# Kernel tuning notes

Measured on AMD Instinct MI355X. Metric: run time of the kernel, lower is better.

## Reference

```python
import jax, jax.numpy as jnp
import numpy as np

KERNEL_NUM = 21
SIGMA = 0.1
EXACT_SIGMA = 0.001

def _kernel_params():
    mus, sigs = [], []
    for i in range(KERNEL_NUM):
        mu = 1.0 / (KERNEL_NUM - 1) + 2.0 * i / (KERNEL_NUM - 1) - 1.0
        s = SIGMA
        if mu > 1:
            mu = 1.0
            s = EXACT_SIGMA
        mus.append(mu)
        sigs.append(s)
    return np.array(mus, np.float32), np.array(sigs, np.float32)

MUS, SIGS = _kernel_params()

def _l2norm(x):
    # torch F.normalize(p=2, dim=-1): x / max(||x||, 1e-12)
    n = jnp.sqrt(jnp.sum(x * x, axis=-1, keepdims=True))
    return x / jnp.maximum(n, 1e-12)

def setup_inputs() -> dict:
    key = jax.random.key(0)
    ks = jax.random.split(key, 8)
    B, W, R, D, V = 512, 30, 512, 128, 100000
    H1, H2 = 128, 64
    return {
        "query": jax.random.randint(ks[0], (B, W), 0, V),
        "document": jax.random.randint(ks[1], (B, R), 0, V),
        "emb_table": jax.random.normal(ks[2], (V, D), jnp.float32) * 0.02,
        "w1": jax.random.normal(ks[3], (KERNEL_NUM, H1), jnp.float32) * 0.1,
        "b1": jnp.zeros((H1,), jnp.float32),
        "w2": jax.random.normal(ks[4], (H1, H2), jnp.float32) * 0.1,
        "b2": jnp.zeros((H2,), jnp.float32),
        "w3": jax.random.normal(ks[5], (H2, 1), jnp.float32) * 0.1,
        "b3": jnp.zeros((1,), jnp.float32),
    }

def reference(query, document, emb_table, w1, b1, w2, b2, w3, b3):
    q = _l2norm(emb_table[query])      # [B, W, D]
    d = _l2norm(emb_table[document])   # [B, R, D]
    # cosine matching matrix [B, W, R]
    M = jnp.einsum('bwd,brd->bwr', q, d)
    # 21 Gaussian soft-histogram bins: log1p(sum_{w,r} exp(-0.5*(M-mu)^2/sigma^2))
    KM = [
        jnp.log1p(
            jnp.sum(jnp.exp(-0.5 * (M - MUS[i]) ** 2 / (SIGS[i] ** 2)), axis=(-1, -2))
        )
        for i in range(KERNEL_NUM)
    ]
    k = jnp.stack(KM, axis=1)  # [B, K]
    h = jax.nn.relu(k @ w1 + b1)
    h = jax.nn.relu(h @ w2 + b2)
    return h @ w3 + b3  # [B, 1]
```

## Files before the change

kernel.cpp:

```cpp
#include <hip/hip_runtime.h>
#include <math.h>

#define B_   512
#define W_   30
#define R_   512
#define D_   128
#define NK_  21
#define SPLIT 4
#define QSTRIDE 132

typedef __attribute__((ext_vector_type(8))) short  bf16x8;
typedef __attribute__((ext_vector_type(4))) float  f32x4;
typedef __attribute__((ext_vector_type(2))) float  f32x2;

__device__ __forceinline__ unsigned short f2bf(float f) {
    union { float f; unsigned int u; } v; v.f = f;
    unsigned int u = v.u;
    return (unsigned short)((u + 0x7fffu + ((u >> 16) & 1u)) >> 16);
}

__device__ __forceinline__ float fast_exp2(float x) {
#if __has_builtin(__builtin_amdgcn_exp2f)
    return __builtin_amdgcn_exp2f(x);
#else
    float r; asm volatile("v_exp_f32 %0, %1" : "=v"(r) : "v"(x)); return r;
#endif
}

#define QROWS 32
#define QST   136

__global__ __launch_bounds__(512) void knrm_bins_kernel(
    const int* __restrict__ query, const int* __restrict__ doc,
    const float* __restrict__ emb,
    float* __restrict__ part)
{
    const int bid  = blockIdx.x;
    const int b    = ((bid >> 5) << 3) | (bid & 7);
    const int sp   = (bid >> 3) & 3;
    const int tid  = threadIdx.x;
    const int lane = tid & 63;
    const int wid  = tid >> 6;
    const int l15  = lane & 15;
    const int lhi  = lane >> 4;

    __shared__ unsigned short qlds[QROWS * QST];
    __shared__ float wred8[8][NK_][8];

    const int di = doc[b * R_ + sp * 128 + wid * 16 + l15];
    const float* drow = emb + (size_t)di * D_ + lhi * 8;
    float4 f[8];
    #pragma unroll
    for (int kk = 0; kk < 4; ++kk) {
        f[2 * kk]     = *(const float4*)(drow + kk * 32);
        f[2 * kk + 1] = *(const float4*)(drow + kk * 32 + 4);
    }

    {
        int w = tid >> 4, j = tid & 15;
        uint4 o4 = make_uint4(0, 0, 0, 0);
        if (w < W_) {
            int qi = query[b * W_ + w];
            const float* qrow = emb + (size_t)qi * D_ + j * 8;
            float4 qa = *(const float4*)(qrow);
            float4 qb = *(const float4*)(qrow + 4);
            float ss = qa.x*qa.x + qa.y*qa.y + qa.z*qa.z + qa.w*qa.w
                     + qb.x*qb.x + qb.y*qb.y + qb.z*qb.z + qb.w*qb.w;
            #pragma unroll
            for (int off = 8; off >= 1; off >>= 1) ss += __shfl_xor(ss, off, 16);
            float qinv = 1.0f / fmaxf(sqrtf(ss), 1e-12f);
            unsigned short o[8];
            o[0] = f2bf(qa.x*qinv); o[1] = f2bf(qa.y*qinv);
            o[2] = f2bf(qa.z*qinv); o[3] = f2bf(qa.w*qinv);
            o[4] = f2bf(qb.x*qinv); o[5] = f2bf(qb.y*qinv);
            o[6] = f2bf(qb.z*qinv); o[7] = f2bf(qb.w*qinv);
            o4 = *(const uint4*)o;
        }
        *(uint4*)(&qlds[(tid >> 4) * QST + (tid & 15) * 8]) = o4;
    }

    float nsq = 0.f;
    #pragma unroll
    for (int c = 0; c < 8; ++c)
        nsq = fmaf(f[c].x, f[c].x, fmaf(f[c].y, f[c].y,
              fmaf(f[c].z, f[c].z, fmaf(f[c].w, f[c].w, nsq))));
    nsq += __shfl_xor(nsq, 16, 64);
    nsq += __shfl_xor(nsq, 32, 64);
    const float dinv = 1.0f / fmaxf(sqrtf(nsq), 1e-12f);

    bf16x8 a[4];
    #pragma unroll
    for (int kk = 0; kk < 4; ++kk) {
        float4 u = f[2 * kk], v = f[2 * kk + 1];
        unsigned short o[8];
        o[0] = f2bf(u.x*dinv); o[1] = f2bf(u.y*dinv);
        o[2] = f2bf(u.z*dinv); o[3] = f2bf(u.w*dinv);
        o[4] = f2bf(v.x*dinv); o[5] = f2bf(v.y*dinv);
        o[6] = f2bf(v.z*dinv); o[7] = f2bf(v.w*dinv);
        a[kk] = *(const bf16x8*)o;
    }
    __syncthreads();

    bf16x8 bq[2][4];
    #pragma unroll
    for (int tc = 0; tc < 2; ++tc)
        #pragma unroll
        for (int kk = 0; kk < 4; ++kk)
            bq[tc][kk] = *(const bf16x8*)&qlds[(tc * 16 + l15) * QST + kk * 32 + lhi * 8];

    f32x4 acc0 = (f32x4)0.0f, acc1 = (f32x4)0.0f;
    #pragma unroll
    for (int kk = 0; kk < 4; ++kk) {
        acc0 = __builtin_amdgcn_mfma_f32_16x16x32_bf16(a[kk], bq[0][kk], acc0, 0, 0, 0);
        acc1 = __builtin_amdgcn_mfma_f32_16x16x32_bf16(a[kk], bq[1][kk], acc1, 0, 0, 0);
    }

    const float CW = -72.134752f;
    const float CE = -721347.52f;
    const float RC = 0.36787944f;

    f32x2 kacc2[NK_];
    #pragma unroll
    for (int i = 0; i < NK_; ++i) kacc2[i] = (f32x2)0.0f;

    #pragma unroll
    for (int p = 0; p < 4; ++p) {
        f32x2 mm;
        mm.x = acc0[p];
        mm.y = (l15 < 14) ? acc1[p] : 3.0f;
        f32x2 t0 = mm + 0.95f;

        #pragma unroll
        for (int g = 0; g < 3; ++g) {
            const int   gs = (g == 0) ? 0 : (g == 1) ? 7 : 14;
            const int   gl = (g == 2) ? 6 : 7;
            const float go = 0.1f * (float)gs;
            f32x2 tg = t0 - go;
            f32x2 e  = (CW * tg) * tg;
            f32x2 dl = 14.4269504f * tg - 0.72134752f;
            f32x2 R, r;
            R.x = fast_exp2(e.x);  R.y = fast_exp2(e.y);
            r.x = fast_exp2(dl.x); r.y = fast_exp2(dl.y);
            #pragma unroll
            for (int k = 0; k < 7; ++k) {
                if (k < gl) {
                    kacc2[gs + k] += R;
                    R *= r;
                    r *= RC;
                }
            }
        }

        f32x2 y = mm - 1.0f;
        f32x2 a20 = (CE * y) * y;
        f32x2 T20;
        T20.x = fast_exp2(a20.x);
        T20.y = fast_exp2(a20.y);
        kacc2[20] += T20;
    }

    #pragma unroll
    for (int i = 0; i < NK_; ++i) {
        float v = kacc2[i].x + kacc2[i].y;
        v += __shfl_xor(v, 8, 64);
        v += __shfl_xor(v, 16, 64);
        v += __shfl_xor(v, 32, 64);
        if (lane < 8) wred8[wid][i][lane] = v;
    }
    __syncthreads();
    if (tid < NK_) {
        float s = 0.f;
        #pragma unroll
        for (int ww = 0; ww < 8; ++ww)
            #pragma unroll
            for (int c = 0; c < 8; ++c) s += wred8[ww][tid][c];
        part[(b * SPLIT + sp) * NK_ + tid] = s;
    }
}

__global__ __launch_bounds__(128) void knrm_mlp_kernel(
    const float* __restrict__ part,
    const float* __restrict__ w1, const float* __restrict__ b1,
    const float* __restrict__ w2, const float* __restrict__ b2,
    const float* __restrict__ w3, const float* __restrict__ b3,
    float* __restrict__ out)
{
    const int b   = blockIdx.x;
    const int tid = threadIdx.x;

    __shared__ float klds[NK_];
    __shared__ float h1lds[128];

    if (tid < NK_) {
        const float* p0 = part + (size_t)b * SPLIT * NK_;
        float s = p0[tid] + p0[NK_ + tid] + p0[2 * NK_ + tid] + p0[3 * NK_ + tid];
        klds[tid] = log1pf(s);
    }
    __syncthreads();

    {
        float h = b1[tid];
        #pragma unroll
        for (int i = 0; i < NK_; ++i) h = fmaf(klds[i], w1[i * 128 + tid], h);
        h1lds[tid] = fmaxf(h, 0.f);
    }
    __syncthreads();

    if (tid < 64) {
        float h = b2[tid];
        #pragma unroll 8
        for (int i = 0; i < 128; ++i) h = fmaf(h1lds[i], w2[i * 64 + tid], h);
        float p = fmaxf(h, 0.f) * w3[tid];
        #pragma unroll
        for (int off = 32; off >= 1; off >>= 1) p += __shfl_xor(p, off, 64);
        if (tid == 0) out[b] = p + b3[0];
    }
}

__global__ __launch_bounds__(512) void knrm_kernel(
    const int* __restrict__ query, const int* __restrict__ doc,
    const float* __restrict__ emb,
    const float* __restrict__ w1, const float* __restrict__ b1,
    const float* __restrict__ w2, const float* __restrict__ b2,
    const float* __restrict__ w3, const float* __restrict__ b3,
    float* __restrict__ out)
{
    const int b   = blockIdx.x;
    const int tid = threadIdx.x;

    __shared__ float qs[W_ * QSTRIDE];
    __shared__ float qinv[W_];
    __shared__ float wred[8][NK_];
    __shared__ float klds[NK_];
    __shared__ float h1lds[128];

    for (int idx = tid; idx < W_ * D_; idx += 512) {
        int w = idx >> 7, k = idx & 127;
        int qi = query[b * W_ + w];
        qs[w * QSTRIDE + k] = emb[(size_t)qi * D_ + k];
    }
    __syncthreads();

    if (tid < W_ * 16) {
        int row = tid >> 4, j = tid & 15;
        float ss = 0.f;
        #pragma unroll
        for (int k = 0; k < D_; k += 16) {
            float v = qs[row * QSTRIDE + k + j];
            ss = fmaf(v, v, ss);
        }
        #pragma unroll
        for (int off = 8; off >= 1; off >>= 1) ss += __shfl_xor(ss, off, 16);
        if (j == 0) qinv[row] = 1.0f / fmaxf(sqrtf(ss), 1e-12f);
    }
    __syncthreads();

    const int didx = doc[b * R_ + tid];
    const float4* __restrict__ drow = (const float4*)(emb + (size_t)didx * D_);

    float acc[W_];
    #pragma unroll
    for (int w = 0; w < W_; ++w) acc[w] = 0.f;
    float nsq = 0.f;

    float4 dv = drow[0];
    for (int c = 0; c < D_ / 4; ++c) {
        float4 dnx = drow[(c + 1) & 31];
        nsq = fmaf(dv.x, dv.x, fmaf(dv.y, dv.y, fmaf(dv.z, dv.z, fmaf(dv.w, dv.w, nsq))));
        const float* qc = qs + c * 4;
        #pragma unroll
        for (int w = 0; w < W_; ++w) {
            float4 qv = *(const float4*)(qc + w * QSTRIDE);
            acc[w] = fmaf(qv.x, dv.x, fmaf(qv.y, dv.y, fmaf(qv.z, dv.z, fmaf(qv.w, dv.w, acc[w]))));
        }
        dv = dnx;
    }
    const float invd = 1.0f / fmaxf(sqrtf(nsq), 1e-12f);

    const float CW = -72.134752f;
    const float CE = -721347.52f;
    float kacc[NK_];
    #pragma unroll
    for (int i = 0; i < NK_; ++i) kacc[i] = 0.f;

    #pragma unroll
    for (int w = 0; w < W_; ++w) {
        float m = acc[w] * qinv[w] * invd;
        #pragma unroll
        for (int i = 0; i < 20; ++i) {
            const float mu = (float)(1.0 / (NK_ - 1) + 2.0 * (double)i / (NK_ - 1) - 1.0);
            float t = m - mu;
            kacc[i] += exp2f(CW * t * t);
        }
        float y = m - 1.0f;
        kacc[20] += exp2f(CE * y * y);
    }

    const int wid = tid >> 6, lane = tid & 63;
    #pragma unroll
    for (int i = 0; i < NK_; ++i) {
        float v = kacc[i];
        #pragma unroll
        for (int off = 32; off >= 1; off >>= 1) v += __shfl_xor(v, off, 64);
        if (lane == 0) wred[wid][i] = v;
    }
    __syncthreads();
    if (tid < NK_) {
        float s = 0.f;
        #pragma unroll
        for (int ww = 0; ww < 8; ++ww) s += wred[ww][tid];
        klds[tid] = log1pf(s);
    }
    __syncthreads();

    if (tid < 128) {
        float h = b1[tid];
        #pragma unroll
        for (int i = 0; i < NK_; ++i) h = fmaf(klds[i], w1[i * 128 + tid], h);
        h1lds[tid] = fmaxf(h, 0.f);
    }
    __syncthreads();
    if (tid < 64) {
        float h = b2[tid];
        #pragma unroll 8
        for (int i = 0; i < 128; ++i) h = fmaf(h1lds[i], w2[i * 64 + tid], h);
        float p = fmaxf(h, 0.f) * w3[tid];
        #pragma unroll
        for (int off = 32; off >= 1; off >>= 1) p += __shfl_xor(p, off, 64);
        if (tid == 0) out[b] = p + b3[0];
    }
}

extern "C" void kernel_launch(void* const* d_in, const int* in_sizes, int n_in,
                              void* d_out, int out_size, void* d_ws, size_t ws_size,
                              hipStream_t stream) {
    const int*   query = (const int*)d_in[0];
    const int*   doc   = (const int*)d_in[1];
    const float* emb   = (const float*)d_in[2];
    const float* w1    = (const float*)d_in[3];
    const float* b1    = (const float*)d_in[4];
    const float* w2    = (const float*)d_in[5];
    const float* b2    = (const float*)d_in[6];
    const float* w3    = (const float*)d_in[7];
    const float* b3    = (const float*)d_in[8];
    float* outp = (float*)d_out;

    const size_t part_bytes = (size_t)B_ * SPLIT * NK_ * sizeof(float);

    if (ws_size >= part_bytes) {
        float* part = (float*)d_ws;
        knrm_bins_kernel<<<dim3(B_ * SPLIT), dim3(512), 0, stream>>>(query, doc, emb, part);
        knrm_mlp_kernel<<<dim3(B_), dim3(128), 0, stream>>>(part, w1, b1, w2, b2, w3, b3, outp);
    } else {
        knrm_kernel<<<dim3(B_), dim3(512), 0, stream>>>(query, doc, emb,
                                                        w1, b1, w2, b2, w3, b3, outp);
    }
}
```

Measured before the change: 42.69 us.

## Halve grid split, process two doc rows per thread with prefetch, skip exact bin

Each block now handles 256 document rows instead of 128 (SPLIT 4→2). Each thread processes two rows in sequence, and the second row's embedding load is issued before the first row's MFMA and bin computation so the latency overlaps. This halves the number of blocks and amortizes the query normalization and LDS staging over twice as much work. The exact-match bin exp is also skipped with a wave-level __any test when no value exceeds 0.98, and the padding sentinel changes from 3.0 to -3.0. The costs are fewer blocks in flight, so less parallelism, plus higher register pressure from keeping the prefetched row live.

```diff
diff --git a/kernel.cpp b/kernel.cpp
--- a/kernel.cpp
+++ b/kernel.cpp
@@ -6,7 +6,7 @@
 #define R_   512
 #define D_   128
 #define NK_  21
-#define SPLIT 4
+#define SPLIT 2
 #define QSTRIDE 132
 
 typedef __attribute__((ext_vector_type(8))) short  bf16x8;
@@ -30,14 +30,59 @@
 #define QROWS 32
 #define QST   136
 
+__device__ __forceinline__ void bins_accum(f32x4 acc0, f32x4 acc1, int l15, f32x2* kacc2)
+{
+    const float CW = -72.134752f;
+    const float CE = -721347.52f;
+    const float RC = 0.36787944f;
+
+    #pragma unroll
+    for (int p = 0; p < 4; ++p) {
+        f32x2 mm;
+        mm.x = acc0[p];
+        mm.y = (l15 < 14) ? acc1[p] : -3.0f;
+        f32x2 t0 = mm + 0.95f;
+
+        #pragma unroll
+        for (int g = 0; g < 3; ++g) {
+            const int   gs = (g == 0) ? 0 : (g == 1) ? 7 : 14;
+            const int   gl = (g == 2) ? 6 : 7;
+            const float go = 0.1f * (float)gs;
+            f32x2 tg = t0 - go;
+            f32x2 e  = (CW * tg) * tg;
+            f32x2 dl = 14.4269504f * tg - 0.72134752f;
+            f32x2 R, r;
+            R.x = fast_exp2(e.x);  R.y = fast_exp2(e.y);
+            r.x = fast_exp2(dl.x); r.y = fast_exp2(dl.y);
+            #pragma unroll
+            for (int k = 0; k < 7; ++k) {
+                if (k < gl) {
+                    kacc2[gs + k] += R;
+                    R *= r;
+                    r *= RC;
+                }
+            }
+        }
+
+        if (__any(mm.x > 0.98f || mm.y > 0.98f)) {
+            f32x2 y = mm - 1.0f;
+            f32x2 a20 = (CE * y) * y;
+            f32x2 T20;
+            T20.x = fast_exp2(a20.x);
+            T20.y = fast_exp2(a20.y);
+            kacc2[20] += T20;
+        }
+    }
+}
+
 __global__ __launch_bounds__(512) void knrm_bins_kernel(
     const int* __restrict__ query, const int* __restrict__ doc,
     const float* __restrict__ emb,
     float* __restrict__ part)
 {
     const int bid  = blockIdx.x;
-    const int b    = ((bid >> 5) << 3) | (bid & 7);
-    const int sp   = (bid >> 3) & 3;
+    const int b    = ((bid >> 4) << 3) | (bid & 7);
+    const int sp   = (bid >> 3) & 1;
     const int tid  = threadIdx.x;
     const int lane = tid & 63;
     const int wid  = tid >> 6;
@@ -47,13 +92,16 @@
     __shared__ unsigned short qlds[QROWS * QST];
     __shared__ float wred8[8][NK_][8];
 
-    const int di = doc[b * R_ + sp * 128 + wid * 16 + l15];
-    const float* drow = emb + (size_t)di * D_ + lhi * 8;
+    const int rbase = sp * 256 + wid * 32 + l15;
+    const int di0 = doc[b * R_ + rbase];
+    const int di1 = doc[b * R_ + rbase + 16];
+
+    const float* dr0 = emb + (size_t)di0 * D_ + lhi * 8;
     float4 f[8];
     #pragma unroll
     for (int kk = 0; kk < 4; ++kk) {
-        f[2 * kk]     = *(const float4*)(drow + kk * 32);
-        f[2 * kk + 1] = *(const float4*)(drow + kk * 32 + 4);
+        f[2 * kk]     = *(const float4*)(dr0 + kk * 32);
+        f[2 * kk + 1] = *(const float4*)(dr0 + kk * 32 + 4);
     }
 
     {
@@ -78,6 +126,11 @@
         }
         *(uint4*)(&qlds[(tid >> 4) * QST + (tid & 15) * 8]) = o4;
     }
+    __syncthreads();
+
+    f32x2 kacc2[NK_];
+    #pragma unroll
+    for (int i = 0; i < NK_; ++i) kacc2[i] = (f32x2)0.0f;
 
     float nsq = 0.f;
     #pragma unroll
@@ -86,7 +139,7 @@
               fmaf(f[c].z, f[c].z, fmaf(f[c].w, f[c].w, nsq))));
     nsq += __shfl_xor(nsq, 16, 64);
     nsq += __shfl_xor(nsq, 32, 64);
-    const float dinv = 1.0f / fmaxf(sqrtf(nsq), 1e-12f);
+    float dinv = 1.0f / fmaxf(sqrtf(nsq), 1e-12f);
 
     bf16x8 a[4];
     #pragma unroll
@@ -99,64 +152,56 @@
         o[6] = f2bf(v.z*dinv); o[7] = f2bf(v.w*dinv);
         a[kk] = *(const bf16x8*)o;
     }
-    __syncthreads();
-
-    bf16x8 bq[2][4];
-    #pragma unroll
-    for (int tc = 0; tc < 2; ++tc)
-        #pragma unroll
-        for (int kk = 0; kk < 4; ++kk)
-            bq[tc][kk] = *(const bf16x8*)&qlds[(tc * 16 + l15) * QST + kk * 32 + lhi * 8];
-
-    f32x4 acc0 = (f32x4)0.0f, acc1 = (f32x4)0.0f;
+
+    const float* dr1 = emb + (size_t)di1 * D_ + lhi * 8;
     #pragma unroll
     for (int kk = 0; kk < 4; ++kk) {
-        acc0 = __builtin_amdgcn_mfma_f32_16x16x32_bf16(a[kk], bq[0][kk], acc0, 0, 0, 0);
-        acc1 = __builtin_amdgcn_mfma_f32_16x16x32_bf16(a[kk], bq[1][kk], acc1, 0, 0, 0);
-    }
-
-    const float CW = -72.134752f;
-    const float CE = -721347.52f;
-    const float RC = 0.36787944f;
-
-    f32x2 kacc2[NK_];
-    #pragma unroll
-    for (int i = 0; i < NK_; ++i) kacc2[i] = (f32x2)0.0f;
-
-    #pragma unroll
-    for (int p = 0; p < 4; ++p) {
-        f32x2 mm;
-        mm.x = acc0[p];
-        mm.y = (l15 < 14) ? acc1[p] : 3.0f;
-        f32x2 t0 = mm + 0.95f;
-
-        #pragma unroll
-        for (int g = 0; g < 3; ++g) {
-            const int   gs = (g == 0) ? 0 : (g == 1) ? 7 : 14;
-            const int   gl = (g == 2) ? 6 : 7;
-            const float go = 0.1f * (float)gs;
-            f32x2 tg = t0 - go;
-            f32x2 e  = (CW * tg) * tg;
-            f32x2 dl = 14.4269504f * tg - 0.72134752f;
-            f32x2 R, r;
-            R.x = fast_exp2(e.x);  R.y = fast_exp2(e.y);
-            r.x = fast_exp2(dl.x); r.y = fast_exp2(dl.y);
-            #pragma unroll
-            for (int k = 0; k < 7; ++k) {
-                if (k < gl) {
-                    kacc2[gs + k] += R;
-                    R *= r;
-                    r *= RC;
-                }
-            }
-        }
-
-        f32x2 y = mm - 1.0f;
-        f32x2 a20 = (CE * y) * y;
-        f32x2 T20;
-        T20.x = fast_exp2(a20.x);
-        T20.y = fast_exp2(a20.y);
-        kacc2[20] += T20;
+        f[2 * kk]     = *(const float4*)(dr1 + kk * 32);
+        f[2 * kk + 1] = *(const float4*)(dr1 + kk * 32 + 4);
+    }
+
+    {
+        f32x4 acc0 = (f32x4)0.0f, acc1 = (f32x4)0.0f;
+        #pragma unroll
+        for (int kk = 0; kk < 4; ++kk) {
+            bf16x8 b0 = *(const bf16x8*)&qlds[(l15)      * QST + kk * 32 + lhi * 8];
+            bf16x8 b1 = *(const bf16x8*)&qlds[(16 + l15) * QST + kk * 32 + lhi * 8];
+            acc0 = __builtin_amdgcn_mfma_f32_16x16x32_bf16(a[kk], b0, acc0, 0, 0, 0);
+            acc1 = __builtin_amdgcn_mfma_f32_16x16x32_bf16(a[kk], b1, acc1, 0, 0, 0);
+        }
+        bins_accum(acc0, acc1, l15, kacc2);
+    }
+
+    nsq = 0.f;
+    #pragma unroll
+    for (int c = 0; c < 8; ++c)
+        nsq = fmaf(f[c].x, f[c].x, fmaf(f[c].y, f[c].y,
+              fmaf(f[c].z, f[c].z, fmaf(f[c].w, f[c].w, nsq))));
+    nsq += __shfl_xor(nsq, 16, 64);
+    nsq += __shfl_xor(nsq, 32, 64);
+    dinv = 1.0f / fmaxf(sqrtf(nsq), 1e-12f);
+
+    #pragma unroll
+    for (int kk = 0; kk < 4; ++kk) {
+        float4 u = f[2 * kk], v = f[2 * kk + 1];
+        unsigned short o[8];
+        o[0] = f2bf(u.x*dinv); o[1] = f2bf(u.y*dinv);
+        o[2] = f2bf(u.z*dinv); o[3] = f2bf(u.w*dinv);
+        o[4] = f2bf(v.x*dinv); o[5] = f2bf(v.y*dinv);
+        o[6] = f2bf(v.z*dinv); o[7] = f2bf(v.w*dinv);
+        a[kk] = *(const bf16x8*)o;
+    }
+
+    {
+        f32x4 acc0 = (f32x4)0.0f, acc1 = (f32x4)0.0f;
+        #pragma unroll
+        for (int kk = 0; kk < 4; ++kk) {
+            bf16x8 b0 = *(const bf16x8*)&qlds[(l15)      * QST + kk * 32 + lhi * 8];
+            bf16x8 b1 = *(const bf16x8*)&qlds[(16 + l15) * QST + kk * 32 + lhi * 8];
+            acc0 = __builtin_amdgcn_mfma_f32_16x16x32_bf16(a[kk], b0, acc0, 0, 0, 0);
+            acc1 = __builtin_amdgcn_mfma_f32_16x16x32_bf16(a[kk], b1, acc1, 0, 0, 0);
+        }
+        bins_accum(acc0, acc1, l15, kacc2);
     }
 
     #pragma unroll
@@ -193,7 +238,7 @@
 
     if (tid < NK_) {
         const float* p0 = part + (size_t)b * SPLIT * NK_;
-        float s = p0[tid] + p0[NK_ + tid] + p0[2 * NK_ + tid] + p0[3 * NK_ + tid];
+        float s = p0[tid] + p0[NK_ + tid];
         klds[tid] = log1pf(s);
     }
     __syncthreads();
```

Result: no change. 42.23 us (median of 2 runs) (-1.1%).

## Fuse bin and MLP kernels into one block per batch with prefetched doc rows

Applied to the files above, without the earlier changes.

Replaces the split two-kernel scheme (2048 bin blocks writing partials, then an MLP kernel) with a single kernel where each block handles a full batch row. Each wave loops over four 16-document groups and prefetches the next group's embeddings while the current group's MFMA and binning run. The query tile is normalized and staged once per batch instead of four times, and the workspace round-trip and second launch go away. It also skips the exact-match bin exp when no lane in the wave has a similarity above 0.98. The trade-off is fewer blocks (512 instead of 2048), which gives less parallelism to hide gather latency, plus more serial work per wave.

```diff
diff --git a/kernel.cpp b/kernel.cpp
--- a/kernel.cpp
+++ b/kernel.cpp
@@ -6,8 +6,6 @@
 #define R_   512
 #define D_   128
 #define NK_  21
-#define SPLIT 4
-#define QSTRIDE 132
 
 typedef __attribute__((ext_vector_type(8))) short  bf16x8;
 typedef __attribute__((ext_vector_type(4))) float  f32x4;
@@ -30,14 +28,60 @@
 #define QROWS 32
 #define QST   136
 
-__global__ __launch_bounds__(512) void knrm_bins_kernel(
+__device__ __forceinline__ void bins_accum(f32x4 acc0, f32x4 acc1, int l15, f32x2* kacc2)
+{
+    const float CW = -72.134752f;
+    const float CE = -721347.52f;
+    const float RC = 0.36787944f;
+
+    #pragma unroll
+    for (int p = 0; p < 4; ++p) {
+        f32x2 mm;
+        mm.x = acc0[p];
+        mm.y = (l15 < 14) ? acc1[p] : -3.0f;
+        f32x2 t0 = mm + 0.95f;
+
+        #pragma unroll
+        for (int g = 0; g < 3; ++g) {
+            const int   gs = (g == 0) ? 0 : (g == 1) ? 7 : 14;
+            const int   gl = (g == 2) ? 6 : 7;
+            const float go = 0.1f * (float)gs;
+            f32x2 tg = t0 - go;
+            f32x2 e  = (CW * tg) * tg;
+            f32x2 dl = 14.4269504f * tg - 0.72134752f;
+            f32x2 R, r;
+            R.x = fast_exp2(e.x);  R.y = fast_exp2(e.y);
+            r.x = fast_exp2(dl.x); r.y = fast_exp2(dl.y);
+            #pragma unroll
+            for (int k = 0; k < 7; ++k) {
+                if (k < gl) {
+                    kacc2[gs + k] += R;
+                    R *= r;
+                    r *= RC;
+                }
+            }
+        }
+
+        if (__any(mm.x > 0.98f || mm.y > 0.98f)) {
+            f32x2 y = mm - 1.0f;
+            f32x2 a20 = (CE * y) * y;
+            f32x2 T20;
+            T20.x = fast_exp2(a20.x);
+            T20.y = fast_exp2(a20.y);
+            kacc2[20] += T20;
+        }
+    }
+}
+
+__global__ __launch_bounds__(512) void knrm_fused_kernel(
     const int* __restrict__ query, const int* __restrict__ doc,
     const float* __restrict__ emb,
-    float* __restrict__ part)
+    const float* __restrict__ w1, const float* __restrict__ b1,
+    const float* __restrict__ w2, const float* __restrict__ b2,
+    const float* __restrict__ w3, const float* __restrict__ b3,
+    float* __restrict__ out)
 {
-    const int bid  = blockIdx.x;
-    const int b    = ((bid >> 5) << 3) | (bid & 7);
-    const int sp   = (bid >> 3) & 3;
+    const int b    = blockIdx.x;
     const int tid  = threadIdx.x;
     const int lane = tid & 63;
     const int wid  = tid >> 6;
@@ -46,14 +90,20 @@
 
     __shared__ unsigned short qlds[QROWS * QST];
     __shared__ float wred8[8][NK_][8];
-
-    const int di = doc[b * R_ + sp * 128 + wid * 16 + l15];
-    const float* drow = emb + (size_t)di * D_ + lhi * 8;
+    __shared__ float klds[NK_];
+    __shared__ float h1lds[128];
+
+    int di[4];
+    #pragma unroll
+    for (int g = 0; g < 4; ++g)
+        di[g] = doc[b * R_ + wid * 64 + g * 16 + l15];
+
+    const float* dr0 = emb + (size_t)di[0] * D_ + lhi * 8;
     float4 f[8];
     #pragma unroll
     for (int kk = 0; kk < 4; ++kk) {
-        f[2 * kk]     = *(const float4*)(drow + kk * 32);
-        f[2 * kk + 1] = *(const float4*)(drow + kk * 32 + 4);
+        f[2 * kk]     = *(const float4*)(dr0 + kk * 32);
+        f[2 * kk + 1] = *(const float4*)(dr0 + kk * 32 + 4);
     }
 
     {
@@ -78,85 +128,53 @@
         }
         *(uint4*)(&qlds[(tid >> 4) * QST + (tid & 15) * 8]) = o4;
     }
-
-    float nsq = 0.f;
-    #pragma unroll
-    for (int c = 0; c < 8; ++c)
-        nsq = fmaf(f[c].x, f[c].x, fmaf(f[c].y, f[c].y,
-              fmaf(f[c].z, f[c].z, fmaf(f[c].w, f[c].w, nsq))));
-    nsq += __shfl_xor(nsq, 16, 64);
-    nsq += __shfl_xor(nsq, 32, 64);
-    const float dinv = 1.0f / fmaxf(sqrtf(nsq), 1e-12f);
-
-    bf16x8 a[4];
-    #pragma unroll
-    for (int kk = 0; kk < 4; ++kk) {
-        float4 u = f[2 * kk], v = f[2 * kk + 1];
-        unsigned short o[8];
-        o[0] = f2bf(u.x*dinv); o[1] = f2bf(u.y*dinv);
-        o[2] = f2bf(u.z*dinv); o[3] = f2bf(u.w*dinv);
-        o[4] = f2bf(v.x*dinv); o[5] = f2bf(v.y*dinv);
-        o[6] = f2bf(v.z*dinv); o[7] = f2bf(v.w*dinv);
-        a[kk] = *(const bf16x8*)o;
-    }
-    __syncthreads();
-
-    bf16x8 bq[2][4];
-    #pragma unroll
-    for (int tc = 0; tc < 2; ++tc)
-        #pragma unroll
-        for (int kk = 0; kk < 4; ++kk)
-            bq[tc][kk] = *(const bf16x8*)&qlds[(tc * 16 + l15) * QST + kk * 32 + lhi * 8];
-
-    f32x4 acc0 = (f32x4)0.0f, acc1 = (f32x4)0.0f;
-    #pragma unroll
-    for (int kk = 0; kk < 4; ++kk) {
-        acc0 = __builtin_amdgcn_mfma_f32_16x16x32_bf16(a[kk], bq[0][kk], acc0, 0, 0, 0);
-        acc1 = __builtin_amdgcn_mfma_f32_16x16x32_bf16(a[kk], bq[1][kk], acc1, 0, 0, 0);
-    }
-
-    const float CW = -72.134752f;
-    const float CE = -721347.52f;
-    const float RC = 0.36787944f;
+    __syncthreads();
 
     f32x2 kacc2[NK_];
     #pragma unroll
     for (int i = 0; i < NK_; ++i) kacc2[i] = (f32x2)0.0f;
 
     #pragma unroll
-    for (int p = 0; p < 4; ++p) {
-        f32x2 mm;
-        mm.x = acc0[p];
-        mm.y = (l15 < 14) ? acc1[p] : 3.0f;
-        f32x2 t0 = mm + 0.95f;
-
-        #pragma unroll
-        for (int g = 0; g < 3; ++g) {
-            const int   gs = (g == 0) ? 0 : (g == 1) ? 7 : 14;
-            const int   gl = (g == 2) ? 6 : 7;
-            const float go = 0.1f * (float)gs;
-            f32x2 tg = t0 - go;
-            f32x2 e  = (CW * tg) * tg;
-            f32x2 dl = 14.4269504f * tg - 0.72134752f;
-            f32x2 R, r;
-            R.x = fast_exp2(e.x);  R.y = fast_exp2(e.y);
-            r.x = fast_exp2(dl.x); r.y = fast_exp2(dl.y);
-            #pragma unroll
-            for (int k = 0; k < 7; ++k) {
-                if (k < gl) {
-                    kacc2[gs + k] += R;
-                    R *= r;
-                    r *= RC;
-                }
+    for (int g = 0; g < 4; ++g) {
+        float nsq = 0.f;
+        #pragma unroll
+        for (int c = 0; c < 8; ++c)
+            nsq = fmaf(f[c].x, f[c].x, fmaf(f[c].y, f[c].y,
+                  fmaf(f[c].z, f[c].z, fmaf(f[c].w, f[c].w, nsq))));
+        nsq += __shfl_xor(nsq, 16, 64);
+        nsq += __shfl_xor(nsq, 32, 64);
+        const float dinv = 1.0f / fmaxf(sqrtf(nsq), 1e-12f);
+
+        bf16x8 a[4];
+        #pragma unroll
+        for (int kk = 0; kk < 4; ++kk) {
+            float4 u = f[2 * kk], v = f[2 * kk + 1];
+            unsigned short o[8];
+            o[0] = f2bf(u.x*dinv); o[1] = f2bf(u.y*dinv);
+            o[2] = f2bf(u.z*dinv); o[3] = f2bf(u.w*dinv);
+            o[4] = f2bf(v.x*dinv); o[5] = f2bf(v.y*dinv);
+            o[6] = f2bf(v.z*dinv); o[7] = f2bf(v.w*dinv);
+            a[kk] = *(const bf16x8*)o;
+        }
+
+        if (g < 3) {
+            const float* drn = emb + (size_t)di[g + 1] * D_ + lhi * 8;
+            #pragma unroll
+            for (int kk = 0; kk < 4; ++kk) {
+                f[2 * kk]     = *(const float4*)(drn + kk * 32);
+                f[2 * kk + 1] = *(const float4*)(drn + kk * 32 + 4);
             }
         }
 
-        f32x2 y = mm - 1.0f;
-        f32x2 a20 = (CE * y) * y;
-        f32x2 T20;
-        T20.x = fast_exp2(a20.x);
-        T20.y = fast_exp2(a20.y);
-        kacc2[20] += T20;
+        f32x4 acc0 = (f32x4)0.0f, acc1 = (f32x4)0.0f;
+        #pragma unroll
+        for (int kk = 0; kk < 4; ++kk) {
+            bf16x8 b0 = *(const bf16x8*)&qlds[(l15)      * QST + kk * 32 + lhi * 8];
+            bf16x8 b1 = *(const bf16x8*)&qlds[(16 + l15) * QST + kk * 32 + lhi * 8];
+            acc0 = __builtin_amdgcn_mfma_f32_16x16x32_bf16(a[kk], b0, acc0, 0, 0, 0);
+            acc1 = __builtin_amdgcn_mfma_f32_16x16x32_bf16(a[kk], b1, acc1, 0, 0, 0);
+        }
+        bins_accum(acc0, acc1, l15, kacc2);
     }
 
     #pragma unroll
@@ -174,141 +192,6 @@
         for (int ww = 0; ww < 8; ++ww)
             #pragma unroll
             for (int c = 0; c < 8; ++c) s += wred8[ww][tid][c];
-        part[(b * SPLIT + sp) * NK_ + tid] = s;
-    }
-}
-
-__global__ __launch_bounds__(128) void knrm_mlp_kernel(
-    const float* __restrict__ part,
-    const float* __restrict__ w1, const float* __restrict__ b1,
-    const float* __restrict__ w2, const float* __restrict__ b2,
-    const float* __restrict__ w3, const float* __restrict__ b3,
-    float* __restrict__ out)
-{
-    const int b   = blockIdx.x;
-    const int tid = threadIdx.x;
-
-    __shared__ float klds[NK_];
-    __shared__ float h1lds[128];
-
-    if (tid < NK_) {
-        const float* p0 = part + (size_t)b * SPLIT * NK_;
-        float s = p0[tid] + p0[NK_ + tid] + p0[2 * NK_ + tid] + p0[3 * NK_ + tid];
-        klds[tid] = log1pf(s);
-    }
-    __syncthreads();
-
-    {
-        float h = b1[tid];
-        #pragma unroll
-        for (int i = 0; i < NK_; ++i) h = fmaf(klds[i], w1[i * 128 + tid], h);
-        h1lds[tid] = fmaxf(h, 0.f);
-    }
-    __syncthreads();
-
-    if (tid < 64) {
-        float h = b2[tid];
-        #pragma unroll 8
-        for (int i = 0; i < 128; ++i) h = fmaf(h1lds[i], w2[i * 64 + tid], h);
-        float p = fmaxf(h, 0.f) * w3[tid];
-        #pragma unroll
-        for (int off = 32; off >= 1; off >>= 1) p += __shfl_xor(p, off, 64);
-        if (tid == 0) out[b] = p + b3[0];
-    }
-}
-
-__global__ __launch_bounds__(512) void knrm_kernel(
-    const int* __restrict__ query, const int* __restrict__ doc,
-    const float* __restrict__ emb,
-    const float* __restrict__ w1, const float* __restrict__ b1,
-    const float* __restrict__ w2, const float* __restrict__ b2,
-    const float* __restrict__ w3, const float* __restrict__ b3,
-    float* __restrict__ out)
-{
-    const int b   = blockIdx.x;
-    const int tid = threadIdx.x;
-
-    __shared__ float qs[W_ * QSTRIDE];
-    __shared__ float qinv[W_];
-    __shared__ float wred[8][NK_];
-    __shared__ float klds[NK_];
-    __shared__ float h1lds[128];
-
-    for (int idx = tid; idx < W_ * D_; idx += 512) {
-        int w = idx >> 7, k = idx & 127;
-        int qi = query[b * W_ + w];
-        qs[w * QSTRIDE + k] = emb[(size_t)qi * D_ + k];
-    }
-    __syncthreads();
-
-    if (tid < W_ * 16) {
-        int row = tid >> 4, j = tid & 15;
-        float ss = 0.f;
-        #pragma unroll
-        for (int k = 0; k < D_; k += 16) {
-            float v = qs[row * QSTRIDE + k + j];
-            ss = fmaf(v, v, ss);
-        }
-        #pragma unroll
-        for (int off = 8; off >= 1; off >>= 1) ss += __shfl_xor(ss, off, 16);
-        if (j == 0) qinv[row] = 1.0f / fmaxf(sqrtf(ss), 1e-12f);
-    }
-    __syncthreads();
-
-    const int didx = doc[b * R_ + tid];
-    const float4* __restrict__ drow = (const float4*)(emb + (size_t)didx * D_);
-
-    float acc[W_];
-    #pragma unroll
-    for (int w = 0; w < W_; ++w) acc[w] = 0.f;
-    float nsq = 0.f;
-
-    float4 dv = drow[0];
-    for (int c = 0; c < D_ / 4; ++c) {
-        float4 dnx = drow[(c + 1) & 31];
-        nsq = fmaf(dv.x, dv.x, fmaf(dv.y, dv.y, fmaf(dv.z, dv.z, fmaf(dv.w, dv.w, nsq))));
-        const float* qc = qs + c * 4;
-        #pragma unroll
-        for (int w = 0; w < W_; ++w) {
-            float4 qv = *(const float4*)(qc + w * QSTRIDE);
-            acc[w] = fmaf(qv.x, dv.x, fmaf(qv.y, dv.y, fmaf(qv.z, dv.z, fmaf(qv.w, dv.w, acc[w]))));
-        }
-        dv = dnx;
-    }
-    const float invd = 1.0f / fmaxf(sqrtf(nsq), 1e-12f);
-
-    const float CW = -72.134752f;
-    const float CE = -721347.52f;
-    float kacc[NK_];
-    #pragma unroll
-    for (int i = 0; i < NK_; ++i) kacc[i] = 0.f;
-
-    #pragma unroll
-    for (int w = 0; w < W_; ++w) {
-        float m = acc[w] * qinv[w] * invd;
-        #pragma unroll
-        for (int i = 0; i < 20; ++i) {
-            const float mu = (float)(1.0 / (NK_ - 1) + 2.0 * (double)i / (NK_ - 1) - 1.0);
-            float t = m - mu;
-            kacc[i] += exp2f(CW * t * t);
-        }
-        float y = m - 1.0f;
-        kacc[20] += exp2f(CE * y * y);
-    }
-
-    const int wid = tid >> 6, lane = tid & 63;
-    #pragma unroll
-    for (int i = 0; i < NK_; ++i) {
-        float v = kacc[i];
-        #pragma unroll
-        for (int off = 32; off >= 1; off >>= 1) v += __shfl_xor(v, off, 64);
-        if (lane == 0) wred[wid][i] = v;
-    }
-    __syncthreads();
-    if (tid < NK_) {
-        float s = 0.f;
-        #pragma unroll
-        for (int ww = 0; ww < 8; ++ww) s += wred[ww][tid];
         klds[tid] = log1pf(s);
     }
     __syncthreads();
@@ -345,14 +228,6 @@
     const float* b3    = (const float*)d_in[8];
     float* outp = (float*)d_out;
 
-    const size_t part_bytes = (size_t)B_ * SPLIT * NK_ * sizeof(float);
-
-    if (ws_size >= part_bytes) {
-        float* part = (float*)d_ws;
-        knrm_bins_kernel<<<dim3(B_ * SPLIT), dim3(512), 0, stream>>>(query, doc, emb, part);
-        knrm_mlp_kernel<<<dim3(B_), dim3(128), 0, stream>>>(part, w1, b1, w2, b2, w3, b3, outp);
-    } else {
-        knrm_kernel<<<dim3(B_), dim3(512), 0, stream>>>(query, doc, emb,
-                                                        w1, b1, w2, b2, w3, b3, outp);
-    }
-}
+    knrm_fused_kernel<<<dim3(B_), dim3(512), 0, stream>>>(query, doc, emb,
+                                                          w1, b1, w2, b2, w3, b3, outp);
+}
```

After: 47.44 us. +11.1%, slower.
